# Kernel optimization log

Measured on AMD Instinct MI355X. Metric: run time of the kernel, lower is better.

Reference implementation:

```python
import jax, jax.numpy as jnp
import numpy as np

B = 4096      # batch of states
N = 32        # SVGD particles per state
D_ACT = 16    # action dim
D_OBS = 64    # obs dim
H = 256       # critic hidden width
STEPS = 3     # num_svgd_steps
LR = 0.1      # svgd_lr
LIMIT = 1.0   # act_limit


def q_mlp(obs, x, w1, b1, w2, b2, w3, b3):
    # SAC-style critic: q(obs, a) -> scalar per row. obs/x: [BN, *]
    h = jnp.concatenate([obs, x], axis=-1)
    h = jax.nn.relu(h @ w1 + b1)
    h = jax.nn.relu(h @ w2 + b2)
    return (h @ w3 + b3)[..., 0]  # [BN]


def rbf_kernel(X, Y):
    # X: [B, N, D] (differentiable), Y: [B, N, D] (detached copy of X)
    diff = X[:, :, None, :] - Y[:, None, :, :]          # [B, N, N, D]
    dist_sq = jnp.sum(diff * diff, axis=-1)             # [B, N, N]
    # median heuristic bandwidth per batch element
    med = jnp.median(dist_sq.reshape(dist_sq.shape[0], -1), axis=-1)
    h = med / np.log(N) + 1e-8
    gamma = jax.lax.stop_gradient(1.0 / (2.0 * h))      # [B]
    K = jnp.exp(-gamma[:, None, None] * dist_sq)        # [B, N, N]
    # dK/dX (grad wrt first argument)
    K_grad = -2.0 * gamma[:, None, None, None] * diff * K[..., None]  # [B,N,N,D]
    return K, diff, gamma, K_grad


def setup_inputs() -> dict:
    key = jax.random.key(0)
    ks = jax.random.split(key, 6)
    BN = B * N
    sc = lambda k, shp: jax.random.normal(k, shp, jnp.float32) * 0.05
    return {
        "obs": jax.random.normal(ks[0], (BN, D_OBS), jnp.float32),
        "a": jax.random.normal(ks[1], (BN, D_ACT), jnp.float32),
        "w1": sc(ks[2], (D_OBS + D_ACT, H)),
        "b1": jnp.zeros((H,), jnp.float32),
        "w2": sc(ks[3], (H, H)),
        "b2": jnp.zeros((H,), jnp.float32),
        "w3": sc(ks[4], (H, 1)),
        "b3": jnp.zeros((1,), jnp.float32),
    }


def reference(obs, a, w1, b1, w2, b2, w3, b3):
    # a0 arrives detached in the original (sampler(obs, a0.detach(), ...))
    a = jax.lax.stop_gradient(a)
    logp = jnp.zeros((B, N), jnp.float32)
    q_fn = lambda X: q_mlp(obs, X, w1, b1, w2, b2, w3, b3)
    q_vals = None
    for _ in range(STEPS):
        # log_prob = min(q1, q1) == q1; score = d(sum q)/dX via vjp
        q_vals, vjp_fn = jax.vjp(q_fn, a)                 # q_vals: [BN]
        score, = vjp_fn(jnp.ones_like(q_vals))            # [BN, D_ACT]
        X = a.reshape(B, N, D_ACT)
        S = score.reshape(B, N, D_ACT)
        K, diff, gamma, K_grad = rbf_kernel(X, jax.lax.stop_gradient(X))
        # phi = (K.detach() @ score - K_grad.sum(2)) / N
        drive = jnp.einsum('bij,bjd->bid', jax.lax.stop_gradient(K), S)
        phi = (drive - K_grad.sum(axis=2)) / N            # [B, N, D]
        # logp correction terms
        tmp1 = (K_grad * S[:, None, :, :]).sum(-1).mean(-1)                 # [B, N]
        tmp2 = -2.0 * gamma[:, None] * (((-K_grad) * diff).sum(-1)
                                        - D_ACT * K).mean(-1)               # [B, N]
        logp = logp - LR * (tmp1 + tmp2)
        # svgd_optim + clamp + detach
        a = a + LR * phi.reshape(B * N, D_ACT)
        a = jax.lax.stop_gradient(jnp.clip(a, -LIMIT, LIMIT))
    return a.reshape(B, N, D_ACT), logp, q_vals
```

## Files before the change

### kernel.cpp

```cpp
#include <hip/hip_runtime.h>
#include <hip/hip_bf16.h>
#include <math.h>

#define BNROWS (4096*32)
#define RB     64
#define LN32   3.4657359027997265f

typedef __attribute__((ext_vector_type(8))) short bf16x8;
typedef __attribute__((ext_vector_type(4))) float f32x4;

static __device__ __forceinline__ ushort f2bf(float x) {
    union { __hip_bfloat16 h; ushort u; } cv;
    cv.h = __float2bfloat16(x);
    return cv.u;
}

__global__ void prep_all(const float* __restrict__ obs,
                         ushort* __restrict__ obs_bf,
                         const float* __restrict__ w1,
                         const float* __restrict__ w2,
                         ushort* __restrict__ pB1, ushort* __restrict__ pB2,
                         ushort* __restrict__ pB3, ushort* __restrict__ pB4) {
    if (blockIdx.x < 8192) {
        size_t i = ((size_t)blockIdx.x * 256 + threadIdx.x) * 4;
        float4 v = *(const float4*)&obs[i];
        ushort4 o;
        o.x = f2bf(v.x); o.y = f2bf(v.y); o.z = f2bf(v.z); o.w = f2bf(v.w);
        *(ushort4*)&obs_bf[i] = o;
        return;
    }
    int g = (blockIdx.x - 8192) * 256 + threadIdx.x;
    ushort out[8];
    ushort* dst;
    if (g < 3072) {
        int lane = g & 63, gc = g >> 6;
        int t = gc / 3, c = gc % 3;
        int m = lane & 15, q = lane >> 4, n = t * 16 + m;
        #pragma unroll
        for (int j = 0; j < 8; ++j) {
            int k = c * 32 + q * 8 + j;
            out[j] = f2bf((k < 80) ? w1[k * 256 + n] : 0.f);
        }
        dst = &pB1[g * 8];
    } else if (g < 11264) {
        int gg = g - 3072;
        int lane = gg & 63, gc = gg >> 6;
        int t = gc >> 3, c = gc & 7;
        int m = lane & 15, q = lane >> 4, n = t * 16 + m;
        #pragma unroll
        for (int j = 0; j < 8; ++j)
            out[j] = f2bf(w2[(c * 32 + q * 8 + j) * 256 + n]);
        dst = &pB2[gg * 8];
    } else if (g < 19456) {
        int gg = g - 11264;
        int lane = gg & 63, gc = gg >> 6;
        int t = gc >> 3, c = gc & 7;
        int m = lane & 15, q = lane >> 4;
        #pragma unroll
        for (int j = 0; j < 8; ++j)
            out[j] = f2bf(w2[(t * 16 + m) * 256 + c * 32 + q * 8 + j]);
        dst = &pB3[gg * 8];
    } else if (g < 19968) {
        int gg = g - 19456;
        int lane = gg & 63, c = gg >> 6;
        int m = lane & 15, q = lane >> 4;
        #pragma unroll
        for (int j = 0; j < 8; ++j)
            out[j] = f2bf(w1[(64 + m) * 256 + c * 32 + q * 8 + j]);
        dst = &pB4[gg * 8];
    } else return;
    *(uint4*)dst = *(uint4*)out;
}

__global__ __launch_bounds__(512) void mlp_mfma(
    const ushort* __restrict__ obs_bf,
    const float* __restrict__ a_in,
    const float* __restrict__ b1,
    const float* __restrict__ b2,
    const float* __restrict__ w3,
    const float* __restrict__ b3,
    const ushort* __restrict__ pB1, const ushort* __restrict__ pB2,
    const ushort* __restrict__ pB3, const ushort* __restrict__ pB4,
    float* __restrict__ score,
    float* __restrict__ qout,
    int wantq)
{
    __shared__ __align__(16) ushort B0[RB * 264];
    __shared__ __align__(16) ushort B1s[RB * 104];
    __shared__ float qpart[8][RB];
    __shared__ float bias1[256], bias2[256], w3s[256];

    const int tid  = threadIdx.x;
    const int row0 = blockIdx.x * RB;

    {
        int r = tid >> 3, ch = tid & 7;
        *(uint4*)&B1s[r * 104 + ch * 8] =
            *(const uint4*)&obs_bf[(size_t)(row0 + r) * 64 + ch * 8];
    }
    if (tid < 256) {
        int r = tid >> 2, d0 = (tid & 3) * 4;
        float4 av = *(const float4*)&a_in[(size_t)(row0 + r) * 16 + d0];
        ushort4 pv;
        pv.x = f2bf(av.x); pv.y = f2bf(av.y); pv.z = f2bf(av.z); pv.w = f2bf(av.w);
        *(ushort4*)&B1s[r * 104 + 64 + d0] = pv;
        ushort4 zv; zv.x = zv.y = zv.z = zv.w = 0;
        *(ushort4*)&B1s[r * 104 + 80 + d0] = zv;
        bias1[tid] = b1[tid]; bias2[tid] = b2[tid]; w3s[tid] = w3[tid];
    }
    __syncthreads();

    const int lane = tid & 63;
    const int w    = tid >> 6;
    const int m    = lane & 15;
    const int q    = lane >> 4;
    const int qk   = q * 8;

    f32x4 acc[4][2];
    unsigned relumask = 0u;

    #pragma unroll
    for (int tc = 0; tc < 2; ++tc)
        #pragma unroll
        for (int rt = 0; rt < 4; ++rt) acc[rt][tc] = (f32x4){0.f, 0.f, 0.f, 0.f};
    for (int c = 0; c < 3; ++c) {
        bf16x8 af[4];
        #pragma unroll
        for (int rt = 0; rt < 4; ++rt)
            af[rt] = *(const bf16x8*)&B1s[(rt * 16 + m) * 104 + c * 32 + qk];
        #pragma unroll
        for (int tc = 0; tc < 2; ++tc) {
            bf16x8 wfr = *(const bf16x8*)&pB1[(((w * 2 + tc) * 3 + c) * 64 + lane) * 8];
            #pragma unroll
            for (int rt = 0; rt < 4; ++rt)
                acc[rt][tc] = __builtin_amdgcn_mfma_f32_16x16x32_bf16(wfr, af[rt], acc[rt][tc], 0, 0, 0);
        }
    }
    #pragma unroll
    for (int tc = 0; tc < 2; ++tc) {
        const float4 bv = *(const float4*)&bias1[(w * 2 + tc) * 16 + q * 4];
        const float bva[4] = {bv.x, bv.y, bv.z, bv.w};
        #pragma unroll
        for (int rt = 0; rt < 4; ++rt) {
            ushort4 pk;
            float z0 = acc[rt][tc][0] + bva[0];
            float z1 = acc[rt][tc][1] + bva[1];
            float z2 = acc[rt][tc][2] + bva[2];
            float z3 = acc[rt][tc][3] + bva[3];
            if (z0 > 0.f) relumask |= 1u << (rt * 8 + tc * 4 + 0);
            if (z1 > 0.f) relumask |= 1u << (rt * 8 + tc * 4 + 1);
            if (z2 > 0.f) relumask |= 1u << (rt * 8 + tc * 4 + 2);
            if (z3 > 0.f) relumask |= 1u << (rt * 8 + tc * 4 + 3);
            pk.x = f2bf(fmaxf(z0, 0.f)); pk.y = f2bf(fmaxf(z1, 0.f));
            pk.z = f2bf(fmaxf(z2, 0.f)); pk.w = f2bf(fmaxf(z3, 0.f));
            *(ushort4*)&B0[(rt * 16 + m) * 264 + (w * 2 + tc) * 16 + q * 4] = pk;
        }
    }
    __syncthreads();

    #pragma unroll
    for (int tc = 0; tc < 2; ++tc)
        #pragma unroll
        for (int rt = 0; rt < 4; ++rt) acc[rt][tc] = (f32x4){0.f, 0.f, 0.f, 0.f};
    for (int c = 0; c < 8; ++c) {
        bf16x8 af[4];
        #pragma unroll
        for (int rt = 0; rt < 4; ++rt)
            af[rt] = *(const bf16x8*)&B0[(rt * 16 + m) * 264 + c * 32 + qk];
        #pragma unroll
        for (int tc = 0; tc < 2; ++tc) {
            bf16x8 wfr = *(const bf16x8*)&pB2[(((w * 2 + tc) * 8 + c) * 64 + lane) * 8];
            #pragma unroll
            for (int rt = 0; rt < 4; ++rt)
                acc[rt][tc] = __builtin_amdgcn_mfma_f32_16x16x32_bf16(wfr, af[rt], acc[rt][tc], 0, 0, 0);
        }
    }
    __syncthreads();
    {
        float qp[4] = {0.f, 0.f, 0.f, 0.f};
        #pragma unroll
        for (int tc = 0; tc < 2; ++tc) {
            const float4 bv = *(const float4*)&bias2[(w * 2 + tc) * 16 + q * 4];
            const float4 wv = *(const float4*)&w3s[(w * 2 + tc) * 16 + q * 4];
            const float bva[4] = {bv.x, bv.y, bv.z, bv.w};
            const float wva[4] = {wv.x, wv.y, wv.z, wv.w};
            #pragma unroll
            for (int rt = 0; rt < 4; ++rt) {
                ushort4 pk; float dz[4];
                #pragma unroll
                for (int i = 0; i < 4; ++i) {
                    float z = acc[rt][tc][i] + bva[i];
                    if (z > 0.f) { qp[rt] += z * wva[i]; dz[i] = wva[i]; }
                    else         { dz[i] = 0.f; }
                }
                pk.x = f2bf(dz[0]); pk.y = f2bf(dz[1]);
                pk.z = f2bf(dz[2]); pk.w = f2bf(dz[3]);
                *(ushort4*)&B0[(rt * 16 + m) * 264 + (w * 2 + tc) * 16 + q * 4] = pk;
            }
        }
        if (wantq) {
            #pragma unroll
            for (int rt = 0; rt < 4; ++rt) {
                float v = qp[rt];
                v += __shfl_xor(v, 16); v += __shfl_xor(v, 32);
                if (q == 0) qpart[w][rt * 16 + m] = v;
            }
        }
    }
    __syncthreads();

    if (wantq && tid < RB) {
        float qs = b3[0];
        #pragma unroll
        for (int ww = 0; ww < 8; ++ww) qs += qpart[ww][tid];
        qout[row0 + tid] = qs;
    }

    #pragma unroll
    for (int tc = 0; tc < 2; ++tc)
        #pragma unroll
        for (int rt = 0; rt < 4; ++rt) acc[rt][tc] = (f32x4){0.f, 0.f, 0.f, 0.f};
    for (int c = 0; c < 8; ++c) {
        bf16x8 af[4];
        #pragma unroll
        for (int rt = 0; rt < 4; ++rt)
            af[rt] = *(const bf16x8*)&B0[(rt * 16 + m) * 264 + c * 32 + qk];
        #pragma unroll
        for (int tc = 0; tc < 2; ++tc) {
            bf16x8 wfr = *(const bf16x8*)&pB3[(((w * 2 + tc) * 8 + c) * 64 + lane) * 8];
            #pragma unroll
            for (int rt = 0; rt < 4; ++rt)
                acc[rt][tc] = __builtin_amdgcn_mfma_f32_16x16x32_bf16(wfr, af[rt], acc[rt][tc], 0, 0, 0);
        }
    }
    __syncthreads();
    #pragma unroll
    for (int rt = 0; rt < 4; ++rt)
        #pragma unroll
        for (int tc = 0; tc < 2; ++tc) {
            ushort4 pk;
            pk.x = f2bf((relumask >> (rt * 8 + tc * 4 + 0)) & 1u ? acc[rt][tc][0] : 0.f);
            pk.y = f2bf((relumask >> (rt * 8 + tc * 4 + 1)) & 1u ? acc[rt][tc][1] : 0.f);
            pk.z = f2bf((relumask >> (rt * 8 + tc * 4 + 2)) & 1u ? acc[rt][tc][2] : 0.f);
            pk.w = f2bf((relumask >> (rt * 8 + tc * 4 + 3)) & 1u ? acc[rt][tc][3] : 0.f);
            *(ushort4*)&B0[(rt * 16 + m) * 264 + (w * 2 + tc) * 16 + q * 4] = pk;
        }
    __syncthreads();

    if (w < 4) {
        f32x4 acc2 = (f32x4){0.f, 0.f, 0.f, 0.f};
        for (int c = 0; c < 8; ++c) {
            bf16x8 af = *(const bf16x8*)&B0[(w * 16 + m) * 264 + c * 32 + qk];
            bf16x8 wfr = *(const bf16x8*)&pB4[(c * 64 + lane) * 8];
            acc2 = __builtin_amdgcn_mfma_f32_16x16x32_bf16(wfr, af, acc2, 0, 0, 0);
        }
        float4 o; o.x = acc2[0]; o.y = acc2[1]; o.z = acc2[2]; o.w = acc2[3];
        *(float4*)&score[(size_t)(row0 + w * 16 + m) * 16 + q * 4] = o;
    }
}

__global__ __launch_bounds__(256, 2) void svgd6(
    const float* __restrict__ a_in,
    const float* __restrict__ score,
    const float* __restrict__ logp_in,
    float* __restrict__ logp_out,
    float* __restrict__ a_out,
    int first)
{
    __shared__ __align__(16) float X4[4][32 * 20];
    __shared__ __align__(16) float S4[4][32 * 20];
    __shared__ __align__(16) float KM4[4][1024];

    const int tid    = threadIdx.x;
    const int wv     = tid >> 6;
    const int lane   = tid & 63;
    const int stateg = blockIdx.x * 4 + wv;
    const size_t base = (size_t)stateg * 512;

    float* X  = X4[wv];
    float* S  = S4[wv];
    float* KM = KM4[wv];

    {
        int g0 = lane * 8;
        int r = g0 >> 4, d0 = g0 & 15;
        float4 va0 = *(const float4*)&a_in[base + g0];
        float4 va1 = *(const float4*)&a_in[base + g0 + 4];
        float4 vs0 = *(const float4*)&score[base + g0];
        float4 vs1 = *(const float4*)&score[base + g0 + 4];
        *(float4*)&X[r * 20 + d0]     = va0;
        *(float4*)&X[r * 20 + d0 + 4] = va1;
        *(float4*)&S[r * 20 + d0]     = vs0;
        *(float4*)&S[r * 20 + d0 + 4] = vs1;
    }
    __asm__ volatile("s_waitcnt lgkmcnt(0)" ::: "memory");

    const int half = lane >> 5;
    const int j    = lane & 31;

    float Xj[16], Sj[16];
    #pragma unroll
    for (int d0 = 0; d0 < 16; d0 += 4) {
        float4 xv = *(const float4*)&X[j * 20 + d0];
        float4 sv = *(const float4*)&S[j * 20 + d0];
        Xj[d0 + 0] = xv.x; Xj[d0 + 1] = xv.y; Xj[d0 + 2] = xv.z; Xj[d0 + 3] = xv.w;
        Sj[d0 + 0] = sv.x; Sj[d0 + 1] = sv.y; Sj[d0 + 2] = sv.z; Sj[d0 + 3] = sv.w;
    }

    unsigned v[16]; float p[16];
    #pragma unroll 4
    for (int t = 0; t < 16; ++t) {
        const float* Xi = &X[(half * 16 + t) * 20];
        float ss = 0.f, pp = 0.f;
        #pragma unroll
        for (int d0 = 0; d0 < 16; d0 += 4) {
            float4 xv = *(const float4*)&Xi[d0];
            float df0 = xv.x - Xj[d0 + 0];
            float df1 = xv.y - Xj[d0 + 1];
            float df2 = xv.z - Xj[d0 + 2];
            float df3 = xv.w - Xj[d0 + 3];
            ss = fmaf(df0, df0, ss); pp = fmaf(df0, Sj[d0 + 0], pp);
            ss = fmaf(df1, df1, ss); pp = fmaf(df1, Sj[d0 + 1], pp);
            ss = fmaf(df2, df2, ss); pp = fmaf(df2, Sj[d0 + 2], pp);
            ss = fmaf(df3, df3, ss); pp = fmaf(df3, Sj[d0 + 3], pp);
        }
        v[t] = __float_as_uint(ss);
        p[t] = pp;
    }

    unsigned vmin, vmax;
    {
        unsigned mn = 0xFFFFFFFFu, mx = 0u;
        #pragma unroll
        for (int t = 0; t < 16; ++t) {
            mn = min(mn, v[t]); mx = max(mx, v[t]);
        }
        #pragma unroll
        for (int off = 1; off < 64; off <<= 1) {
            mn = min(mn, (unsigned)__shfl_xor((int)mn, off));
            mx = max(mx, (unsigned)__shfl_xor((int)mx, off));
        }
        vmin = mn; vmax = mx;
    }
    unsigned lo = vmin, hi = vmax;
    while (lo < hi) {
        unsigned mid = lo + ((hi - lo) >> 1);
        int c = 0;
        #pragma unroll
        for (int t = 0; t < 16; ++t) c += (v[t] <= mid) ? 1 : 0;
        #pragma unroll
        for (int off = 1; off < 64; off <<= 1) c += __shfl_xor(c, off);
        if (c >= 512) hi = mid; else lo = mid + 1;
    }
    const unsigned prefix = lo;
    const float v1 = __uint_as_float(prefix);

    int cle = 0;
    unsigned mgt = 0xFFFFFFFFu;
    #pragma unroll
    for (int t = 0; t < 16; ++t) {
        if (v[t] <= prefix) cle++;
        else mgt = min(mgt, v[t]);
    }
    #pragma unroll
    for (int off = 1; off < 64; off <<= 1) {
        cle += __shfl_xor(cle, off);
        mgt = min(mgt, (unsigned)__shfl_xor((int)mgt, off));
    }
    const float v2  = (cle >= 513) ? v1 : __uint_as_float(mgt);
    const float med = 0.5f * (v1 + v2);
    const float gamma = 1.0f / (2.0f * (med / LN32 + 1e-8f));

    #pragma unroll 4
    for (int t = 0; t < 16; ++t) {
        int i = half * 16 + t;
        float kk = __expf(-gamma * __uint_as_float(v[t]));
        KM[i * 32 + (j ^ i)] = kk;
        float acc = fmaf(fmaf(2.f * gamma, __uint_as_float(v[t]), -16.f), kk,
                         kk * p[t]);
        #pragma unroll
        for (int off = 1; off < 32; off <<= 1)
            acc += __shfl_xor(acc, off);
        if (j == 0) {
            float tmp = -2.f * gamma * acc * (1.f / 32.f);
            float prev = first ? 0.f : logp_in[stateg * 32 + i];
            logp_out[stateg * 32 + i] = prev - 0.1f * tmp;
        }
    }
    __asm__ volatile("s_waitcnt lgkmcnt(0)" ::: "memory");

    {
        const int d  = lane & 15;
        const int i0 = lane >> 4;
        float s1[8], s2[8], xi[8];
        #pragma unroll
        for (int e = 0; e < 8; ++e) {
            s1[e] = 0.f; s2[e] = 0.f;
            xi[e] = X[(i0 + 4 * e) * 20 + d];
        }
        for (int jj = 0; jj < 32; ++jj) {
            float xjv = X[jj * 20 + d];
            float sjv = S[jj * 20 + d];
            #pragma unroll
            for (int e = 0; e < 8; ++e) {
                int i = i0 + 4 * e;
                float kk = KM[i * 32 + (jj ^ i)];
                s1[e] = fmaf(kk, sjv, s1[e]);
                s2[e] = fmaf(kk, xi[e] - xjv, s2[e]);
            }
        }
        #pragma unroll
        for (int e = 0; e < 8; ++e) {
            int i = i0 + 4 * e;
            float phi = (s1[e] + 2.f * gamma * s2[e]) * (1.f / 32.f);
            float av = xi[e] + 0.1f * phi;
            av = fminf(fmaxf(av, -1.f), 1.f);
            a_out[base + i * 16 + d] = av;
        }
    }
}

extern "C" void kernel_launch(void* const* d_in, const int* in_sizes, int n_in,
                              void* d_out, int out_size, void* d_ws, size_t ws_size,
                              hipStream_t stream) {
    const float* obs = (const float*)d_in[0];
    const float* a0  = (const float*)d_in[1];
    const float* w1  = (const float*)d_in[2];
    const float* b1  = (const float*)d_in[3];
    const float* w2  = (const float*)d_in[4];
    const float* b2  = (const float*)d_in[5];
    const float* w3  = (const float*)d_in[6];
    const float* b3  = (const float*)d_in[7];

    float* out_a    = (float*)d_out;
    float* out_logp = out_a + (size_t)BNROWS * 16;
    float* out_q    = out_logp + BNROWS;

    char* p = (char*)d_ws;
    ushort* pB1 = (ushort*)p; p += 24576 * 2;
    ushort* pB2 = (ushort*)p; p += 65536 * 2;
    ushort* pB3 = (ushort*)p; p += 65536 * 2;
    ushort* pB4 = (ushort*)p; p += 4096 * 2;
    ushort* obs_bf = (ushort*)p; p += (size_t)BNROWS * 64 * 2;
    float* abuf0 = (float*)p; p += (size_t)BNROWS * 16 * 4;
    float* abuf1 = (float*)p; p += (size_t)BNROWS * 16 * 4;
    float* scr   = (float*)p; p += (size_t)BNROWS * 16 * 4;
    float* logp  = (float*)p; p += (size_t)BNROWS * 4;
    float* qtmp  = (float*)p;

    prep_all<<<8270, 256, 0, stream>>>(obs, obs_bf, w1, w2, pB1, pB2, pB3, pB4);

    const int MB = BNROWS / RB;
    const int SB = 4096 / 4;

    mlp_mfma<<<MB, 512, 0, stream>>>(obs_bf, a0, b1, b2, w3, b3,
                                     pB1, pB2, pB3, pB4, scr, qtmp, 0);
    svgd6<<<SB, 256, 0, stream>>>(a0, scr, nullptr, logp, abuf0, 1);
    mlp_mfma<<<MB, 512, 0, stream>>>(obs_bf, abuf0, b1, b2, w3, b3,
                                     pB1, pB2, pB3, pB4, scr, qtmp, 0);
    svgd6<<<SB, 256, 0, stream>>>(abuf0, scr, logp, logp, abuf1, 0);
    mlp_mfma<<<MB, 512, 0, stream>>>(obs_bf, abuf1, b1, b2, w3, b3,
                                     pB1, pB2, pB3, pB4, scr, out_q, 1);
    svgd6<<<SB, 256, 0, stream>>>(abuf1, scr, logp, out_logp, out_a, 0);
}
```

Baseline: 326.8 us.

## Store MLP activations in MFMA fragment-order LDS layout and read obs directly

Replaces the padded row-major LDS activation buffers with a fragment-ordered layout, so each lane's bf16x8 operand is one contiguous 16-byte read at lane*8. The obs part of layer 1 is now loaded straight from global memory into registers rather than staged through LDS, and only the action columns are staged. Biases and w3 are read from global memory instead of being copied into LDS. This cuts LDS footprint and staging work, and should lower bank conflicts on fragment reads. The trade-off is more scattered 8-byte stores when writing activations, and uncoalesced-style global reads for obs and biases.

Result: slower. 370.5 us (+13.4%).

```diff
diff --git a/kernel.cpp b/kernel.cpp
--- a/kernel.cpp
+++ b/kernel.cpp
@@ -85,36 +85,29 @@
     float* __restrict__ qout,
     int wantq)
 {
-    __shared__ __align__(16) ushort B0[RB * 264];
-    __shared__ __align__(16) ushort B1s[RB * 104];
+    __shared__ __align__(16) ushort AF[4 * 8 * 64 * 8];
+    __shared__ __align__(16) ushort BaF[4 * 64 * 8];
     __shared__ float qpart[8][RB];
-    __shared__ float bias1[256], bias2[256], w3s[256];
 
     const int tid  = threadIdx.x;
     const int row0 = blockIdx.x * RB;
-
-    {
-        int r = tid >> 3, ch = tid & 7;
-        *(uint4*)&B1s[r * 104 + ch * 8] =
-            *(const uint4*)&obs_bf[(size_t)(row0 + r) * 64 + ch * 8];
-    }
-    if (tid < 256) {
-        int r = tid >> 2, d0 = (tid & 3) * 4;
-        float4 av = *(const float4*)&a_in[(size_t)(row0 + r) * 16 + d0];
-        ushort4 pv;
-        pv.x = f2bf(av.x); pv.y = f2bf(av.y); pv.z = f2bf(av.z); pv.w = f2bf(av.w);
-        *(ushort4*)&B1s[r * 104 + 64 + d0] = pv;
-        ushort4 zv; zv.x = zv.y = zv.z = zv.w = 0;
-        *(ushort4*)&B1s[r * 104 + 80 + d0] = zv;
-        bias1[tid] = b1[tid]; bias2[tid] = b2[tid]; w3s[tid] = w3[tid];
-    }
-    __syncthreads();
-
     const int lane = tid & 63;
     const int w    = tid >> 6;
     const int m    = lane & 15;
     const int q    = lane >> 4;
-    const int qk   = q * 8;
+
+    if (tid < 256) {
+        int r = tid >> 2, d0 = (tid & 3) * 4;
+        int rt = r >> 4, mm = r & 15;
+        float4 av = *(const float4*)&a_in[(size_t)(row0 + r) * 16 + d0];
+        ushort4 pv;
+        pv.x = f2bf(av.x); pv.y = f2bf(av.y); pv.z = f2bf(av.z); pv.w = f2bf(av.w);
+        int qp_ = d0 >> 3, j0 = d0 & 7;
+        *(ushort4*)&BaF[((rt * 64 + qp_ * 16 + mm) << 3) + j0] = pv;
+        ushort4 zv; zv.x = zv.y = zv.z = zv.w = 0;
+        *(ushort4*)&BaF[((rt * 64 + (2 + qp_) * 16 + mm) << 3) + j0] = zv;
+    }
+    __syncthreads();
 
     f32x4 acc[4][2];
     unsigned relumask = 0u;
@@ -123,11 +116,12 @@
     for (int tc = 0; tc < 2; ++tc)
         #pragma unroll
         for (int rt = 0; rt < 4; ++rt) acc[rt][tc] = (f32x4){0.f, 0.f, 0.f, 0.f};
-    for (int c = 0; c < 3; ++c) {
+    #pragma unroll
+    for (int c = 0; c < 2; ++c) {
         bf16x8 af[4];
         #pragma unroll
         for (int rt = 0; rt < 4; ++rt)
-            af[rt] = *(const bf16x8*)&B1s[(rt * 16 + m) * 104 + c * 32 + qk];
+            af[rt] = *(const bf16x8*)&obs_bf[(size_t)(row0 + rt * 16 + m) * 64 + c * 32 + q * 8];
         #pragma unroll
         for (int tc = 0; tc < 2; ++tc) {
             bf16x8 wfr = *(const bf16x8*)&pB1[(((w * 2 + tc) * 3 + c) * 64 + lane) * 8];
@@ -136,9 +130,26 @@
                 acc[rt][tc] = __builtin_amdgcn_mfma_f32_16x16x32_bf16(wfr, af[rt], acc[rt][tc], 0, 0, 0);
         }
     }
+    {
+        bf16x8 af[4];
+        #pragma unroll
+        for (int rt = 0; rt < 4; ++rt)
+            af[rt] = *(const bf16x8*)&BaF[(rt * 64 + lane) * 8];
+        #pragma unroll
+        for (int tc = 0; tc < 2; ++tc) {
+            bf16x8 wfr = *(const bf16x8*)&pB1[(((w * 2 + tc) * 3 + 2) * 64 + lane) * 8];
+            #pragma unroll
+            for (int rt = 0; rt < 4; ++rt)
+                acc[rt][tc] = __builtin_amdgcn_mfma_f32_16x16x32_bf16(wfr, af[rt], acc[rt][tc], 0, 0, 0);
+        }
+    }
     #pragma unroll
     for (int tc = 0; tc < 2; ++tc) {
-        const float4 bv = *(const float4*)&bias1[(w * 2 + tc) * 16 + q * 4];
+        const int tile = w * 2 + tc;
+        const int kblk = tile >> 1;
+        const int koff = ((tile & 1) << 4) + q * 4;
+        const int qp_  = koff >> 3, j0 = koff & 7;
+        const float4 bv = *(const float4*)&b1[tile * 16 + q * 4];
         const float bva[4] = {bv.x, bv.y, bv.z, bv.w};
         #pragma unroll
         for (int rt = 0; rt < 4; ++rt) {
@@ -153,7 +164,7 @@
             if (z3 > 0.f) relumask |= 1u << (rt * 8 + tc * 4 + 3);
             pk.x = f2bf(fmaxf(z0, 0.f)); pk.y = f2bf(fmaxf(z1, 0.f));
             pk.z = f2bf(fmaxf(z2, 0.f)); pk.w = f2bf(fmaxf(z3, 0.f));
-            *(ushort4*)&B0[(rt * 16 + m) * 264 + (w * 2 + tc) * 16 + q * 4] = pk;
+            *(ushort4*)&AF[(((rt * 8 + kblk) * 64 + qp_ * 16 + m) << 3) + j0] = pk;
         }
     }
     __syncthreads();
@@ -166,7 +177,7 @@
         bf16x8 af[4];
         #pragma unroll
         for (int rt = 0; rt < 4; ++rt)
-            af[rt] = *(const bf16x8*)&B0[(rt * 16 + m) * 264 + c * 32 + qk];
+            af[rt] = *(const bf16x8*)&AF[((rt * 8 + c) * 64 + lane) * 8];
         #pragma unroll
         for (int tc = 0; tc < 2; ++tc) {
             bf16x8 wfr = *(const bf16x8*)&pB2[(((w * 2 + tc) * 8 + c) * 64 + lane) * 8];
@@ -180,8 +191,12 @@
         float qp[4] = {0.f, 0.f, 0.f, 0.f};
         #pragma unroll
         for (int tc = 0; tc < 2; ++tc) {
-            const float4 bv = *(const float4*)&bias2[(w * 2 + tc) * 16 + q * 4];
-            const float4 wv = *(const float4*)&w3s[(w * 2 + tc) * 16 + q * 4];
+            const int tile = w * 2 + tc;
+            const int kblk = tile >> 1;
+            const int koff = ((tile & 1) << 4) + q * 4;
+            const int qp_  = koff >> 3, j0 = koff & 7;
+            const float4 bv = *(const float4*)&b2[tile * 16 + q * 4];
+            const float4 wv = *(const float4*)&w3[tile * 16 + q * 4];
             const float bva[4] = {bv.x, bv.y, bv.z, bv.w};
             const float wva[4] = {wv.x, wv.y, wv.z, wv.w};
             #pragma unroll
@@ -195,7 +210,7 @@
                 }
                 pk.x = f2bf(dz[0]); pk.y = f2bf(dz[1]);
                 pk.z = f2bf(dz[2]); pk.w = f2bf(dz[3]);
-                *(ushort4*)&B0[(rt * 16 + m) * 264 + (w * 2 + tc) * 16 + q * 4] = pk;
+                *(ushort4*)&AF[(((rt * 8 + kblk) * 64 + qp_ * 16 + m) << 3) + j0] = pk;
             }
         }
         if (wantq) {
@@ -224,7 +239,7 @@
         bf16x8 af[4];
         #pragma unroll
         for (int rt = 0; rt < 4; ++rt)
-            af[rt] = *(const bf16x8*)&B0[(rt * 16 + m) * 264 + c * 32 + qk];
+            af[rt] = *(const bf16x8*)&AF[((rt * 8 + c) * 64 + lane) * 8];
         #pragma unroll
         for (int tc = 0; tc < 2; ++tc) {
             bf16x8 wfr = *(const bf16x8*)&pB3[(((w * 2 + tc) * 8 + c) * 64 + lane) * 8];
@@ -235,22 +250,27 @@
     }
     __syncthreads();
     #pragma unroll
-    for (int rt = 0; rt < 4; ++rt)
-        #pragma unroll
-        for (int tc = 0; tc < 2; ++tc) {
+    for (int tc = 0; tc < 2; ++tc) {
+        const int tile = w * 2 + tc;
+        const int kblk = tile >> 1;
+        const int koff = ((tile & 1) << 4) + q * 4;
+        const int qp_  = koff >> 3, j0 = koff & 7;
+        #pragma unroll
+        for (int rt = 0; rt < 4; ++rt) {
             ushort4 pk;
             pk.x = f2bf((relumask >> (rt * 8 + tc * 4 + 0)) & 1u ? acc[rt][tc][0] : 0.f);
             pk.y = f2bf((relumask >> (rt * 8 + tc * 4 + 1)) & 1u ? acc[rt][tc][1] : 0.f);
             pk.z = f2bf((relumask >> (rt * 8 + tc * 4 + 2)) & 1u ? acc[rt][tc][2] : 0.f);
             pk.w = f2bf((relumask >> (rt * 8 + tc * 4 + 3)) & 1u ? acc[rt][tc][3] : 0.f);
-            *(ushort4*)&B0[(rt * 16 + m) * 264 + (w * 2 + tc) * 16 + q * 4] = pk;
-        }
+            *(ushort4*)&AF[(((rt * 8 + kblk) * 64 + qp_ * 16 + m) << 3) + j0] = pk;
+        }
+    }
     __syncthreads();
 
     if (w < 4) {
         f32x4 acc2 = (f32x4){0.f, 0.f, 0.f, 0.f};
         for (int c = 0; c < 8; ++c) {
-            bf16x8 af = *(const bf16x8*)&B0[(w * 16 + m) * 264 + c * 32 + qk];
+            bf16x8 af = *(const bf16x8*)&AF[((w * 8 + c) * 64 + lane) * 8];
             bf16x8 wfr = *(const bf16x8*)&pB4[(c * 64 + lane) * 8];
             acc2 = __builtin_amdgcn_mfma_f32_16x16x32_bf16(wfr, af, acc2, 0, 0, 0);
         }
```
